# Kernel optimization log

Hardware: AMD Instinct MI355X
Metric: run time of the kernel (lower is better)

Reference implementation:

```python
import jax, jax.numpy as jnp
import numpy as np

B, S, D = 4, 2048, 2048
H, K = 16, 128          # num_heads, intermediate_dim
FINAL = H * K           # 2048
VDIM = 2048             # vector_dim
EPS_LN = 1e-6
EPS_NORM = 1e-30


def setup_inputs() -> dict:
    key = jax.random.key(0)
    ks = jax.random.split(key, 8)
    x = jax.random.normal(ks[0], (B, S, D), dtype=jnp.float32)
    vector = jax.random.normal(ks[1], (B, VDIM), dtype=jnp.float32)
    W_att = jax.random.normal(ks[2], (D, H), dtype=jnp.float32) / np.sqrt(D)
    temperature = jnp.ones((1, 1, H), dtype=jnp.float32)
    W_values = jax.random.normal(ks[3], (D, H, K), dtype=jnp.float32) / np.sqrt(D)
    W_op = jax.random.normal(ks[4], (FINAL, VDIM), dtype=jnp.float32) / np.sqrt(FINAL)
    ff1 = jax.random.normal(ks[5], (VDIM + D, D), dtype=jnp.float32) / np.sqrt(VDIM + D)
    ff1_b = jnp.zeros((1, 1, D), dtype=jnp.float32)
    ff2 = jax.random.normal(ks[6], (D, D), dtype=jnp.float32) / np.sqrt(D)
    ff2_b = jnp.zeros((1, 1, D), dtype=jnp.float32)
    gamma = jnp.ones((D,), dtype=jnp.float32)
    beta = jnp.zeros((D,), dtype=jnp.float32)
    return {"x": x, "vector": vector, "W_att": W_att, "temperature": temperature,
            "W_values": W_values, "W_op": W_op, "ff1": ff1, "ff1_b": ff1_b,
            "ff2": ff2, "ff2_b": ff2_b, "gamma": gamma, "beta": beta}


def reference(x, vector, W_att, temperature, W_values, W_op, ff1, ff1_b, ff2, ff2_b, gamma, beta):
    b, s, d = x.shape
    # attention gate per (query) position -- [B,S,H]
    logits = jnp.matmul(x, W_att)
    logits = logits - jnp.max(logits, axis=-2, keepdims=True)
    w = jnp.exp(logits * temperature)
    # exact collapse of repeat+tril+normalize: A[b,i,j,h] = w[b,i,h]*tril[i,j]
    # denom[b,i,h] = w[b,i,h]*(i+1) + 1e-30  ->  out = coef * causal cumsum of v
    counts = jnp.arange(1, s + 1, dtype=x.dtype)[None, :, None]  # [1,S,1]
    coef = w / (w * counts + EPS_NORM)                            # [B,S,H]
    v = jnp.einsum('bsi,ihk->bshk', x, W_values)                  # [B,S,H,K]
    cum_v = jnp.cumsum(v, axis=1)                                 # prefix-sum over keys
    pooled = (coef[..., None] * cum_v).reshape(b, s, -1)          # [B,S,H*K]
    op = jnp.matmul(pooled, W_op) + vector[:, None, :]            # [B,S,VDIM]
    concat = jnp.concatenate([x, op], axis=-1)                    # [B,S,VDIM+D]
    h = jax.nn.relu(jnp.matmul(concat, ff1) + ff1_b)
    h = jax.nn.relu(jnp.matmul(h, ff2) + ff2_b)
    res = h + x
    mean = jnp.mean(res, axis=-1, keepdims=True)
    cen = res - mean
    var = jnp.mean(cen * cen, axis=-1, keepdims=True)
    return cen / jnp.sqrt(var + EPS_LN) * gamma + beta
```

## Files before the change

### kernel.cpp

```cpp
#include <hip/hip_runtime.h>
#include <stdint.h>

#define B_DIM 4
#define S_DIM 2048
#define D_DIM 2048
#define H_DIM 16
#define M_ROWS (B_DIM * S_DIM)
#define CONCAT_LD 4096
#define NCHUNK 32
#define CHLEN (S_DIM / NCHUNK)

#define BM 128
#define BN 128
#define BK 64

typedef __attribute__((ext_vector_type(8))) __bf16 bf16x8;
typedef __attribute__((ext_vector_type(4))) float f32x4;

__device__ inline unsigned short f2bf(float f) {
  union { float f; unsigned u; } x; x.f = f;
  unsigned r = x.u + 0x7fffu + ((x.u >> 16) & 1u);
  return (unsigned short)(r >> 16);
}
__device__ inline float bf2f(unsigned short s) {
  union { unsigned u; float f; } x; x.u = ((unsigned)s) << 16;
  return x.f;
}

__global__ __launch_bounds__(256) void xconv_logits_kernel(
    const float* __restrict__ x, const float* __restrict__ Watt,
    unsigned short* __restrict__ concat, float* __restrict__ logits) {
  int row = blockIdx.x, t = threadIdx.x;
  const float* xr = x + (size_t)row * D_DIM;
  unsigned short* cr = concat + (size_t)row * CONCAT_LD;
  float p[H_DIM];
#pragma unroll
  for (int h = 0; h < H_DIM; ++h) p[h] = 0.f;
#pragma unroll
  for (int i = 0; i < 8; ++i) {
    int k = t + i * 256;
    float xv = xr[k];
    cr[k] = f2bf(xv);
    const float* wr = Watt + (size_t)k * H_DIM;
#pragma unroll
    for (int h = 0; h < H_DIM; ++h) p[h] += xv * wr[h];
  }
  __shared__ float red[4][H_DIM];
  int l = t & 63, w = t >> 6;
#pragma unroll
  for (int h = 0; h < H_DIM; ++h) {
    float v = p[h];
    for (int off = 32; off; off >>= 1) v += __shfl_down(v, off);
    if (l == 0) red[w][h] = v;
  }
  __syncthreads();
  if (t < H_DIM)
    logits[(size_t)row * H_DIM + t] = red[0][t] + red[1][t] + red[2][t] + red[3][t];
}

__global__ __launch_bounds__(256) void prep_kernel(
    const float* __restrict__ Wval, const float* __restrict__ ff1,
    const float* __restrict__ ff2, const float* __restrict__ Wop,
    unsigned short* __restrict__ wv_t, unsigned short* __restrict__ btff1,
    unsigned short* __restrict__ f1bT, unsigned short* __restrict__ ff2_t,
    unsigned short* __restrict__ wop_bf) {
  int z = blockIdx.z;
  if (z == 4) {
    size_t idx = (((size_t)blockIdx.y * 64 + blockIdx.x) * 256 + threadIdx.x) * 4;
    const float4 v = *(const float4*)(Wop + idx);
    ushort4 o;
    o.x = f2bf(v.x); o.y = f2bf(v.y); o.z = f2bf(v.z); o.w = f2bf(v.w);
    *(ushort4*)(wop_bf + idx) = o;
    return;
  }
  const float* src;
  unsigned short* dst;
  int ldd;
  if (z == 0)      { src = Wval;                        dst = wv_t;  ldd = 2048; }
  else if (z == 1) { src = ff1;                         dst = btff1; ldd = 4096; }
  else if (z == 2) { src = ff1 + (size_t)2048 * 2048;   dst = f1bT;  ldd = 2048; }
  else             { src = ff2;                         dst = ff2_t; ldd = 2048; }
  __shared__ float tile[32][33];
  int c0 = blockIdx.x * 32, r0 = blockIdx.y * 32;
  int tx = threadIdx.x & 31, ty = threadIdx.x >> 5;
#pragma unroll
  for (int i = 0; i < 32; i += 8)
    tile[ty + i][tx] = src[(size_t)(r0 + ty + i) * 2048 + c0 + tx];
  __syncthreads();
#pragma unroll
  for (int i = 0; i < 32; i += 8)
    dst[(size_t)(c0 + ty + i) * ldd + r0 + tx] = f2bf(tile[tx][ty + i]);
}

__global__ __launch_bounds__(256) void coef_kernel(
    const float* __restrict__ logits, const float* __restrict__ temp, float* __restrict__ coef) {
  int b = blockIdx.x >> 4, h = blockIdx.x & 15;
  int t = threadIdx.x;
  const float* lg = logits + (size_t)b * S_DIM * H_DIM + h;
  float mx = -1e30f;
  for (int s = t; s < S_DIM; s += 256) mx = fmaxf(mx, lg[(size_t)s * H_DIM]);
  for (int off = 32; off; off >>= 1) mx = fmaxf(mx, __shfl_down(mx, off));
  __shared__ float red[4];
  if ((t & 63) == 0) red[t >> 6] = mx;
  __syncthreads();
  mx = fmaxf(fmaxf(red[0], red[1]), fmaxf(red[2], red[3]));
  float T = temp[h];
  float* cf = coef + (size_t)b * S_DIM * H_DIM + h;
  for (int s = t; s < S_DIM; s += 256) {
    float w = expf((lg[(size_t)s * H_DIM] - mx) * T);
    cf[(size_t)s * H_DIM] = w / (w * (float)(s + 1) + 1e-30f);
  }
}

__global__ __launch_bounds__(256) void bias2_partial_kernel(
    const float* __restrict__ vector, const float* __restrict__ ff1,
    float* __restrict__ part) {
  int n = blockIdx.x * 256 + threadIdx.x;
  int seg = blockIdx.y, b = blockIdx.z;
  const float* vr = vector + (size_t)b * 2048 + seg * 128;
  const float* fr = ff1 + (size_t)(2048 + seg * 128) * 2048 + n;
  float acc = 0.f;
#pragma unroll 8
  for (int j = 0; j < 128; ++j) acc += vr[j] * fr[(size_t)j * 2048];
  part[((size_t)seg * 4 + b) * 2048 + n] = acc;
}

__global__ __launch_bounds__(256) void bias2_reduce_kernel(
    const float* __restrict__ part, const float* __restrict__ ff1_b,
    float* __restrict__ bias2) {
  int n = blockIdx.x * 256 + threadIdx.x;
  int b = blockIdx.y;
  float acc = ff1_b[n];
#pragma unroll
  for (int s = 0; s < 16; ++s) acc += part[((size_t)s * 4 + b) * 2048 + n];
  bias2[(size_t)b * 2048 + n] = acc;
}

template <int MODE>
__global__ __launch_bounds__(256) void gemm_bt_kernel(
    const unsigned short* __restrict__ A, int lda,
    const unsigned short* __restrict__ Bt, int ldb, int K,
    void* __restrict__ outp, int ldo,
    const float* __restrict__ bias, const float* __restrict__ resid) {
  __shared__ unsigned short As[BM * BK];
  __shared__ unsigned short Bs[BN * BK];
  const int t = threadIdx.x;
  const int w = t >> 6, l = t & 63;
  const int wm = w & 1, wn = w >> 1;
  const int q = l >> 4, ln = l & 15;

  const int L = blockIdx.y * 16 + blockIdx.x;
  const int xcd = L & 7;
  const int W = L >> 3;
  const int bx = W & 15;
  const int by = (W >> 4) * 8 + xcd;
  const int m0 = by * BM, n0 = bx * BN;

  f32x4 acc[4][4];
#pragma unroll
  for (int i = 0; i < 4; ++i)
#pragma unroll
    for (int j = 0; j < 4; ++j) acc[i][j] = {0.f, 0.f, 0.f, 0.f};

  for (int k0 = 0; k0 < K; k0 += BK) {
    __syncthreads();
#pragma unroll
    for (int r = 0; r < 4; ++r) {
      int s = r * 256 + t;
      int row = s >> 3;
      int ch = (s & 7) ^ (row & 7);
      const unsigned short* ga = A + (size_t)(m0 + row) * lda + k0 + ch * 8;
      __builtin_amdgcn_global_load_lds(
          (const __attribute__((address_space(1))) void*)ga,
          (__attribute__((address_space(3))) void*)(As + (r * 256 + w * 64) * 8), 16, 0, 0);
      const unsigned short* gb = Bt + (size_t)(n0 + row) * ldb + k0 + ch * 8;
      __builtin_amdgcn_global_load_lds(
          (const __attribute__((address_space(1))) void*)gb,
          (__attribute__((address_space(3))) void*)(Bs + (r * 256 + w * 64) * 8), 16, 0, 0);
    }
    __syncthreads();
#pragma unroll
    for (int h = 0; h < 2; ++h) {
      bf16x8 af[4], bfr[4];
#pragma unroll
      for (int mt = 0; mt < 4; ++mt) {
        int ar = wm * 64 + mt * 16 + ln;
        af[mt] = *(const bf16x8*)&As[ar * BK + (((h * 4 + q) ^ (ar & 7)) * 8)];
      }
#pragma unroll
      for (int nt = 0; nt < 4; ++nt) {
        int br = wn * 64 + nt * 16 + ln;
        bfr[nt] = *(const bf16x8*)&Bs[br * BK + (((h * 4 + q) ^ (br & 7)) * 8)];
      }
#pragma unroll
      for (int mt = 0; mt < 4; ++mt)
#pragma unroll
        for (int nt = 0; nt < 4; ++nt)
          acc[mt][nt] = __builtin_amdgcn_mfma_f32_16x16x32_bf16(af[mt], bfr[nt], acc[mt][nt], 0, 0, 0);
    }
  }

#pragma unroll
  for (int mt = 0; mt < 4; ++mt) {
#pragma unroll
    for (int i = 0; i < 4; ++i) {
      int row = m0 + wm * 64 + mt * 16 + q * 4 + i;
#pragma unroll
      for (int nt = 0; nt < 4; ++nt) {
        int col = n0 + wn * 64 + nt * 16 + ln;
        float vv = acc[mt][nt][i];
        if (MODE == 2) { vv += bias[(size_t)(row >> 11) * 2048 + col]; vv = fmaxf(vv, 0.f); }
        if (MODE == 4) {
          vv += bias[col]; vv = fmaxf(vv, 0.f);
          vv += resid[(size_t)row * 2048 + col];
          ((float*)outp)[(size_t)row * ldo + col] = vv;
        } else {
          ((unsigned short*)outp)[(size_t)row * ldo + col] = f2bf(vv);
        }
      }
    }
  }
}

#define GLD16(g, s)                                                        \
  __builtin_amdgcn_global_load_lds(                                        \
      (const __attribute__((address_space(1))) void*)(g),                  \
      (__attribute__((address_space(3))) void*)(s), 16, 0, 0)
#define BARX() asm volatile("s_barrier" ::: "memory")
#define VMW8() asm volatile("s_waitcnt vmcnt(8)" ::: "memory")
#define VMW4() asm volatile("s_waitcnt vmcnt(4)" ::: "memory")
#define VMW0() asm volatile("s_waitcnt vmcnt(0)" ::: "memory")

template <int MODE>
__global__ __launch_bounds__(512, 2) void gemm256_kernel(
    const unsigned short* __restrict__ A, int lda,
    const unsigned short* __restrict__ Bt, int ldb, int K,
    void* __restrict__ outp, int ldo,
    const float* __restrict__ bias, const float* __restrict__ resid) {
  __shared__ unsigned short As[2][2][256 * 32];
  __shared__ unsigned short Bs[2][2][256 * 32];
  const int t = threadIdx.x;
  const int wv = t >> 6, l = t & 63;
  const int wm = wv >> 2, wn = wv & 3;
  const int q = l >> 4, ln = l & 15;

  const int L = blockIdx.y * 8 + blockIdx.x;
  const int lin = (L & 7) * 32 + (L >> 3);
  const int m0 = (lin >> 3) * 256, n0 = (lin & 7) * 256;

  const int srow = t >> 2;
  const int scol = (((t & 3) * 16) ^ (((srow >> 1) & 3) << 4)) >> 1;
  const unsigned short* Abase = A + (size_t)(m0 + srow) * lda + scol;
  const unsigned short* Bbase = Bt + (size_t)(n0 + srow) * ldb + scol;
  const size_t astep = (size_t)128 * lda, bstep = (size_t)128 * ldb;
  const int rsel = (q * 8) ^ (((ln >> 1) & 3) << 3);

  f32x4 acc[8][4];
#pragma unroll
  for (int i = 0; i < 8; ++i)
#pragma unroll
    for (int j = 0; j < 4; ++j) acc[i][j] = {0.f, 0.f, 0.f, 0.f};

  auto stageA = [&](int kt, int kh, int buf) {
    const unsigned short* g = Abase + (size_t)kt * 64 + kh * 32;
    GLD16(g, &As[buf][kh][wv * 512]);
    GLD16(g + astep, &As[buf][kh][4096 + wv * 512]);
  };
  auto stageB = [&](int kt, int kh, int buf) {
    const unsigned short* g = Bbase + (size_t)kt * 64 + kh * 32;
    GLD16(g, &Bs[buf][kh][wv * 512]);
    GLD16(g + bstep, &Bs[buf][kh][4096 + wv * 512]);
  };

  bf16x8 a[8], b[2];
  auto loadA = [&](int buf, int h) {
#pragma unroll
    for (int mt = 0; mt < 8; ++mt) {
      int ar = wm * 128 + mt * 16 + ln;
      a[mt] = *(const bf16x8*)&As[buf][h][ar * 32 + rsel];
    }
  };
  auto loadB2 = [&](int buf, int h, int np) {
#pragma unroll
    for (int i = 0; i < 2; ++i) {
      int br = wn * 64 + (np * 2 + i) * 16 + ln;
      b[i] = *(const bf16x8*)&Bs[buf][h][br * 32 + rsel];
    }
  };
  auto mm = [&](int np) {
    __builtin_amdgcn_s_setprio(1);
#pragma unroll
    for (int mt = 0; mt < 8; ++mt)
#pragma unroll
      for (int i = 0; i < 2; ++i)
        acc[mt][np * 2 + i] =
            __builtin_amdgcn_mfma_f32_16x16x32_bf16(a[mt], b[i], acc[mt][np * 2 + i], 0, 0, 0);
    __builtin_amdgcn_s_setprio(0);
  };

  const int NT = K >> 6;
  stageA(0, 0, 0); stageB(0, 0, 0);
  stageA(0, 1, 0); stageB(0, 1, 0);
  stageA(1, 0, 1); stageB(1, 0, 1);
  VMW4();
  BARX();

  for (int tt = 0; tt < NT; ++tt) {
    const int c = tt & 1;
    const int t1 = (tt + 1 == NT) ? 0 : tt + 1;
    const int t2 = (tt + 2 >= NT) ? tt + 2 - NT : tt + 2;
    loadA(c, 0); loadB2(c, 0, 0);
    stageA(t1, 1, c ^ 1);
    BARX();
    mm(0);
    BARX();
    loadB2(c, 0, 1);
    stageB(t1, 1, c ^ 1);
    BARX();
    mm(1);
    VMW8();
    BARX();
    loadA(c, 1); loadB2(c, 1, 0);
    stageA(t2, 0, c);
    BARX();
    mm(0);
    BARX();
    loadB2(c, 1, 1);
    stageB(t2, 0, c);
    BARX();
    mm(1);
    VMW8();
    BARX();
  }
  VMW0();

#pragma unroll
  for (int mt = 0; mt < 8; ++mt) {
#pragma unroll
    for (int i = 0; i < 4; ++i) {
      int row = m0 + wm * 128 + mt * 16 + q * 4 + i;
#pragma unroll
      for (int nt = 0; nt < 4; ++nt) {
        int col = n0 + wn * 64 + nt * 16 + ln;
        float vv = acc[mt][nt][i];
        if (MODE == 2) { vv += bias[(size_t)(row >> 11) * 2048 + col]; vv = fmaxf(vv, 0.f); }
        if (MODE == 4) {
          vv += bias[col]; vv = fmaxf(vv, 0.f);
          vv += resid[(size_t)row * 2048 + col];
          ((float*)outp)[(size_t)row * ldo + col] = vv;
        } else {
          ((unsigned short*)outp)[(size_t)row * ldo + col] = f2bf(vv);
        }
      }
    }
  }
}

__global__ __launch_bounds__(256) void scan_partial_kernel(
    const unsigned short* __restrict__ v, float* __restrict__ csum) {
  int c = blockIdx.x * 256 + threadIdx.x;
  int chunk = blockIdx.y, b = blockIdx.z;
  const unsigned short* p = v + ((size_t)(b * S_DIM + chunk * CHLEN)) * D_DIM + c;
  float s = 0.f;
#pragma unroll 4
  for (int i = 0; i < CHLEN; ++i) s += bf2f(p[(size_t)i * D_DIM]);
  csum[((size_t)b * NCHUNK + chunk) * D_DIM + c] = s;
}

__global__ __launch_bounds__(256) void scan_apply_kernel(
    const unsigned short* __restrict__ v, const float* __restrict__ csum,
    const float* __restrict__ coef, unsigned short* __restrict__ pooled_out) {
  int c = blockIdx.x * 256 + threadIdx.x;
  int chunk = blockIdx.y, b = blockIdx.z;
  int h = c >> 7;
  int row0 = b * S_DIM + chunk * CHLEN;
  const float* cs = csum + (size_t)b * NCHUNK * D_DIM + c;
  float run = 0.f;
  for (int j = 0; j < chunk; ++j) run += cs[(size_t)j * D_DIM];
  const unsigned short* vp = v + (size_t)row0 * D_DIM + c;
  unsigned short* po = pooled_out + (size_t)row0 * CONCAT_LD + c;
  const float* cf = coef + (size_t)row0 * H_DIM + h;
#pragma unroll 4
  for (int i = 0; i < CHLEN; ++i) {
    run += bf2f(vp[(size_t)i * D_DIM]);
    po[(size_t)i * CONCAT_LD] = f2bf(cf[(size_t)i * H_DIM] * run);
  }
}

__global__ __launch_bounds__(256) void ln_kernel(
    float* __restrict__ out, const float* __restrict__ gamma, const float* __restrict__ beta) {
  int row = blockIdx.x, t = threadIdx.x;
  float* pr = out + (size_t)row * D_DIM;
  float vals[8];
  float s = 0.f;
#pragma unroll
  for (int i = 0; i < 8; ++i) { vals[i] = pr[t + i * 256]; s += vals[i]; }
  __shared__ float red[4];
  for (int off = 32; off; off >>= 1) s += __shfl_down(s, off);
  if ((t & 63) == 0) red[t >> 6] = s;
  __syncthreads();
  float mean = (red[0] + red[1] + red[2] + red[3]) * (1.f / D_DIM);
  __syncthreads();
  float c2 = 0.f;
#pragma unroll
  for (int i = 0; i < 8; ++i) { float c = vals[i] - mean; c2 += c * c; }
  for (int off = 32; off; off >>= 1) c2 += __shfl_down(c2, off);
  if ((t & 63) == 0) red[t >> 6] = c2;
  __syncthreads();
  float var = (red[0] + red[1] + red[2] + red[3]) * (1.f / D_DIM);
  float rstd = rsqrtf(var + 1e-6f);
#pragma unroll
  for (int i = 0; i < 8; ++i) {
    int col = t + i * 256;
    pr[col] = (vals[i] - mean) * rstd * gamma[col] + beta[col];
  }
}

extern "C" void kernel_launch(void* const* d_in, const int* in_sizes, int n_in,
                              void* d_out, int out_size, void* d_ws, size_t ws_size,
                              hipStream_t stream) {
  const float* x      = (const float*)d_in[0];
  const float* vector = (const float*)d_in[1];
  const float* W_att  = (const float*)d_in[2];
  const float* temp   = (const float*)d_in[3];
  const float* W_val  = (const float*)d_in[4];
  const float* W_op   = (const float*)d_in[5];
  const float* ff1    = (const float*)d_in[6];
  const float* ff1_b  = (const float*)d_in[7];
  const float* ff2    = (const float*)d_in[8];
  const float* ff2_b  = (const float*)d_in[9];
  const float* gamma  = (const float*)d_in[10];
  const float* beta   = (const float*)d_in[11];
  float* out = (float*)d_out;

  char* ws = (char*)d_ws;
  auto alloc = [&](size_t bytes) {
    char* p = ws; ws += (bytes + 255) & ~(size_t)255; return p;
  };
  unsigned short* concat = (unsigned short*)alloc((size_t)M_ROWS * CONCAT_LD * 2);
  unsigned short* wv_t   = (unsigned short*)alloc((size_t)2048 * 2048 * 2);
  unsigned short* btff1  = (unsigned short*)alloc((size_t)2048 * 4096 * 2);
  unsigned short* f1bT   = (unsigned short*)alloc((size_t)2048 * 2048 * 2);
  unsigned short* wop_bf = (unsigned short*)alloc((size_t)2048 * 2048 * 2);
  unsigned short* ff2_t  = (unsigned short*)alloc((size_t)2048 * 2048 * 2);
  unsigned short* vbuf   = (unsigned short*)alloc((size_t)M_ROWS * 2048 * 2);
  unsigned short* h1     = (unsigned short*)alloc((size_t)M_ROWS * 2048 * 2);
  float* logits = (float*)alloc((size_t)M_ROWS * H_DIM * 4);
  float* coef   = (float*)alloc((size_t)M_ROWS * H_DIM * 4);
  float* csum   = (float*)alloc((size_t)B_DIM * NCHUNK * D_DIM * 4);
  float* part   = (float*)alloc((size_t)16 * 4 * 2048 * 4);
  float* bias2  = (float*)alloc((size_t)4 * 2048 * 4);

  prep_kernel<<<dim3(64, 64, 5), 256, 0, stream>>>(
      W_val, ff1, ff2, W_op, wv_t, btff1, f1bT, ff2_t, wop_bf);
  xconv_logits_kernel<<<M_ROWS, 256, 0, stream>>>(x, W_att, concat, logits);
  coef_kernel<<<B_DIM * H_DIM, 256, 0, stream>>>(logits, temp, coef);
  gemm_bt_kernel<1><<<dim3(16, 16), 256, 0, stream>>>(
      f1bT, 2048, wop_bf, 2048, 2048, btff1 + 2048, 4096, nullptr, nullptr);
  bias2_partial_kernel<<<dim3(8, 16, 4), 256, 0, stream>>>(vector, ff1, part);
  bias2_reduce_kernel<<<dim3(8, 4), 256, 0, stream>>>(part, ff1_b, bias2);
  gemm256_kernel<1><<<dim3(8, 32), 512, 0, stream>>>(
      concat, CONCAT_LD, wv_t, 2048, 2048, vbuf, 2048, nullptr, nullptr);
  scan_partial_kernel<<<dim3(8, NCHUNK, B_DIM), 256, 0, stream>>>(vbuf, csum);
  scan_apply_kernel<<<dim3(8, NCHUNK, B_DIM), 256, 0, stream>>>(vbuf, csum, coef, concat + 2048);
  gemm256_kernel<2><<<dim3(8, 32), 512, 0, stream>>>(
      concat, CONCAT_LD, btff1, 4096, 4096, h1, 2048, bias2, nullptr);
  gemm256_kernel<4><<<dim3(8, 32), 512, 0, stream>>>(
      h1, 2048, ff2_t, 2048, 2048, out, 2048, ff2_b, x);
  ln_kernel<<<M_ROWS, 256, 0, stream>>>(out, gamma, beta);
}
```

Measured before the change: 651.4 us.

## Vectorize memory access in elementwise, scan, transpose and layernorm kernels

Widens global loads and stores across the auxiliary kernels. The x-conversion/logits kernel now handles four rows per block with float4 loads and reuses each W_att row across them. The transpose prep writes ushort2 pairs over 64-row tiles, and the scan kernels process eight bf16 columns per thread with 128-bit accesses and twice as many chunks. Layernorm uses float4 loads and stores. The aim is to cut memory-instruction count and uncoalesced narrow accesses in these bandwidth-bound steps, at the cost of fewer blocks in the scans and more registers per thread.

```diff
diff --git a/kernel.cpp b/kernel.cpp
--- a/kernel.cpp
+++ b/kernel.cpp
@@ -7,7 +7,7 @@
 #define H_DIM 16
 #define M_ROWS (B_DIM * S_DIM)
 #define CONCAT_LD 4096
-#define NCHUNK 32
+#define NCHUNK 64
 #define CHLEN (S_DIM / NCHUNK)
 
 #define BM 128
@@ -26,36 +26,63 @@
   union { unsigned u; float f; } x; x.u = ((unsigned)s) << 16;
   return x.f;
 }
+__device__ inline float bfLo(unsigned u) {
+  union { unsigned x; float f; } c; c.x = u << 16; return c.f;
+}
+__device__ inline float bfHi(unsigned u) {
+  union { unsigned x; float f; } c; c.x = u & 0xffff0000u; return c.f;
+}
 
 __global__ __launch_bounds__(256) void xconv_logits_kernel(
     const float* __restrict__ x, const float* __restrict__ Watt,
     unsigned short* __restrict__ concat, float* __restrict__ logits) {
-  int row = blockIdx.x, t = threadIdx.x;
-  const float* xr = x + (size_t)row * D_DIM;
-  unsigned short* cr = concat + (size_t)row * CONCAT_LD;
-  float p[H_DIM];
-#pragma unroll
-  for (int h = 0; h < H_DIM; ++h) p[h] = 0.f;
-#pragma unroll
-  for (int i = 0; i < 8; ++i) {
-    int k = t + i * 256;
-    float xv = xr[k];
-    cr[k] = f2bf(xv);
-    const float* wr = Watt + (size_t)k * H_DIM;
-#pragma unroll
-    for (int h = 0; h < H_DIM; ++h) p[h] += xv * wr[h];
-  }
-  __shared__ float red[4][H_DIM];
+  int r0 = blockIdx.x * 4, t = threadIdx.x;
+  float p[4][H_DIM];
+#pragma unroll
+  for (int r = 0; r < 4; ++r)
+#pragma unroll
+    for (int h = 0; h < H_DIM; ++h) p[r][h] = 0.f;
+#pragma unroll
+  for (int i = 0; i < 2; ++i) {
+    int k = t * 4 + i * 1024;
+    float4 xv[4];
+#pragma unroll
+    for (int r = 0; r < 4; ++r) {
+      xv[r] = *(const float4*)(x + (size_t)(r0 + r) * D_DIM + k);
+      ushort4 o;
+      o.x = f2bf(xv[r].x); o.y = f2bf(xv[r].y); o.z = f2bf(xv[r].z); o.w = f2bf(xv[r].w);
+      *(ushort4*)(concat + (size_t)(r0 + r) * CONCAT_LD + k) = o;
+    }
+#pragma unroll
+    for (int kk = 0; kk < 4; ++kk) {
+      const float* w = Watt + (size_t)(k + kk) * H_DIM;
+      float wr[H_DIM];
+#pragma unroll
+      for (int h = 0; h < H_DIM; ++h) wr[h] = w[h];
+#pragma unroll
+      for (int r = 0; r < 4; ++r) {
+        float xs = (kk == 0) ? xv[r].x : (kk == 1) ? xv[r].y : (kk == 2) ? xv[r].z : xv[r].w;
+#pragma unroll
+        for (int h = 0; h < H_DIM; ++h) p[r][h] += xs * wr[h];
+      }
+    }
+  }
+  __shared__ float red[4][4][H_DIM];
   int l = t & 63, w = t >> 6;
 #pragma unroll
-  for (int h = 0; h < H_DIM; ++h) {
-    float v = p[h];
-    for (int off = 32; off; off >>= 1) v += __shfl_down(v, off);
-    if (l == 0) red[w][h] = v;
-  }
+  for (int r = 0; r < 4; ++r)
+#pragma unroll
+    for (int h = 0; h < H_DIM; ++h) {
+      float v = p[r][h];
+      for (int off = 32; off; off >>= 1) v += __shfl_down(v, off);
+      if (l == 0) red[w][r][h] = v;
+    }
   __syncthreads();
-  if (t < H_DIM)
-    logits[(size_t)row * H_DIM + t] = red[0][t] + red[1][t] + red[2][t] + red[3][t];
+  if (t < 64) {
+    int r = t >> 4, h = t & 15;
+    logits[(size_t)(r0 + r) * H_DIM + h] =
+        red[0][r][h] + red[1][r][h] + red[2][r][h] + red[3][r][h];
+  }
 }
 
 __global__ __launch_bounds__(256) void prep_kernel(
@@ -64,13 +91,16 @@
     unsigned short* __restrict__ wv_t, unsigned short* __restrict__ btff1,
     unsigned short* __restrict__ f1bT, unsigned short* __restrict__ ff2_t,
     unsigned short* __restrict__ wop_bf) {
-  int z = blockIdx.z;
+  int z = blockIdx.z, t = threadIdx.x;
   if (z == 4) {
-    size_t idx = (((size_t)blockIdx.y * 64 + blockIdx.x) * 256 + threadIdx.x) * 4;
-    const float4 v = *(const float4*)(Wop + idx);
-    ushort4 o;
-    o.x = f2bf(v.x); o.y = f2bf(v.y); o.z = f2bf(v.z); o.w = f2bf(v.w);
-    *(ushort4*)(wop_bf + idx) = o;
+    size_t idx = (((size_t)blockIdx.y * 64 + blockIdx.x) * 256 + t) * 8;
+    const float4 v0 = *(const float4*)(Wop + idx);
+    const float4 v1 = *(const float4*)(Wop + idx + 4);
+    ushort4 a, b;
+    a.x = f2bf(v0.x); a.y = f2bf(v0.y); a.z = f2bf(v0.z); a.w = f2bf(v0.w);
+    b.x = f2bf(v1.x); b.y = f2bf(v1.y); b.z = f2bf(v1.z); b.w = f2bf(v1.w);
+    *(ushort4*)(wop_bf + idx) = a;
+    *(ushort4*)(wop_bf + idx + 4) = b;
     return;
   }
   const float* src;
@@ -80,16 +110,22 @@
   else if (z == 1) { src = ff1;                         dst = btff1; ldd = 4096; }
   else if (z == 2) { src = ff1 + (size_t)2048 * 2048;   dst = f1bT;  ldd = 2048; }
   else             { src = ff2;                         dst = ff2_t; ldd = 2048; }
-  __shared__ float tile[32][33];
-  int c0 = blockIdx.x * 32, r0 = blockIdx.y * 32;
-  int tx = threadIdx.x & 31, ty = threadIdx.x >> 5;
-#pragma unroll
-  for (int i = 0; i < 32; i += 8)
+  __shared__ float tile[64][33];
+  int c0 = blockIdx.x * 32, r0 = blockIdx.y * 64;
+  int tx = t & 31, ty = t >> 5;
+#pragma unroll
+  for (int i = 0; i < 64; i += 8)
     tile[ty + i][tx] = src[(size_t)(r0 + ty + i) * 2048 + c0 + tx];
   __syncthreads();
-#pragma unroll
-  for (int i = 0; i < 32; i += 8)
-    dst[(size_t)(c0 + ty + i) * ldd + r0 + tx] = f2bf(tile[tx][ty + i]);
+  int sx = t & 31, sy = t >> 5;
+#pragma unroll
+  for (int j = 0; j < 32; j += 8) {
+    int c = c0 + sy + j;
+    ushort2 o;
+    o.x = f2bf(tile[sx * 2][sy + j]);
+    o.y = f2bf(tile[sx * 2 + 1][sy + j]);
+    *(ushort2*)(dst + (size_t)c * ldd + r0 + sx * 2) = o;
+  }
 }
 
 __global__ __launch_bounds__(256) void coef_kernel(
@@ -358,32 +394,57 @@
 
 __global__ __launch_bounds__(256) void scan_partial_kernel(
     const unsigned short* __restrict__ v, float* __restrict__ csum) {
-  int c = blockIdx.x * 256 + threadIdx.x;
-  int chunk = blockIdx.y, b = blockIdx.z;
-  const unsigned short* p = v + ((size_t)(b * S_DIM + chunk * CHLEN)) * D_DIM + c;
-  float s = 0.f;
-#pragma unroll 4
-  for (int i = 0; i < CHLEN; ++i) s += bf2f(p[(size_t)i * D_DIM]);
-  csum[((size_t)b * NCHUNK + chunk) * D_DIM + c] = s;
+  int chunk = blockIdx.x, b = blockIdx.y;
+  int c0 = threadIdx.x * 8;
+  const unsigned short* p = v + ((size_t)(b * S_DIM + chunk * CHLEN)) * D_DIM + c0;
+  float s[8];
+#pragma unroll
+  for (int j = 0; j < 8; ++j) s[j] = 0.f;
+  for (int i = 0; i < CHLEN; ++i) {
+    uint4 u = *(const uint4*)(p + (size_t)i * D_DIM);
+    s[0] += bfLo(u.x); s[1] += bfHi(u.x);
+    s[2] += bfLo(u.y); s[3] += bfHi(u.y);
+    s[4] += bfLo(u.z); s[5] += bfHi(u.z);
+    s[6] += bfLo(u.w); s[7] += bfHi(u.w);
+  }
+  float* cs = csum + ((size_t)b * NCHUNK + chunk) * D_DIM + c0;
+  float4 o0 = {s[0], s[1], s[2], s[3]}, o1 = {s[4], s[5], s[6], s[7]};
+  *(float4*)cs = o0;
+  *(float4*)(cs + 4) = o1;
 }
 
 __global__ __launch_bounds__(256) void scan_apply_kernel(
     const unsigned short* __restrict__ v, const float* __restrict__ csum,
     const float* __restrict__ coef, unsigned short* __restrict__ pooled_out) {
-  int c = blockIdx.x * 256 + threadIdx.x;
-  int chunk = blockIdx.y, b = blockIdx.z;
-  int h = c >> 7;
+  int chunk = blockIdx.x, b = blockIdx.y;
+  int c0 = threadIdx.x * 8;
+  const float* cs = csum + (size_t)b * NCHUNK * D_DIM + c0;
+  float run[8];
+#pragma unroll
+  for (int j = 0; j < 8; ++j) run[j] = 0.f;
+  for (int j = 0; j < chunk; ++j) {
+    float4 a = *(const float4*)(cs + (size_t)j * D_DIM);
+    float4 d = *(const float4*)(cs + (size_t)j * D_DIM + 4);
+    run[0] += a.x; run[1] += a.y; run[2] += a.z; run[3] += a.w;
+    run[4] += d.x; run[5] += d.y; run[6] += d.z; run[7] += d.w;
+  }
   int row0 = b * S_DIM + chunk * CHLEN;
-  const float* cs = csum + (size_t)b * NCHUNK * D_DIM + c;
-  float run = 0.f;
-  for (int j = 0; j < chunk; ++j) run += cs[(size_t)j * D_DIM];
-  const unsigned short* vp = v + (size_t)row0 * D_DIM + c;
-  unsigned short* po = pooled_out + (size_t)row0 * CONCAT_LD + c;
-  const float* cf = coef + (size_t)row0 * H_DIM + h;
-#pragma unroll 4
+  const unsigned short* vp = v + (size_t)row0 * D_DIM + c0;
+  unsigned short* po = pooled_out + (size_t)row0 * CONCAT_LD + c0;
+  const float* cf = coef + (size_t)row0 * H_DIM + (c0 >> 7);
   for (int i = 0; i < CHLEN; ++i) {
-    run += bf2f(vp[(size_t)i * D_DIM]);
-    po[(size_t)i * CONCAT_LD] = f2bf(cf[(size_t)i * H_DIM] * run);
+    uint4 u = *(const uint4*)(vp + (size_t)i * D_DIM);
+    run[0] += bfLo(u.x); run[1] += bfHi(u.x);
+    run[2] += bfLo(u.y); run[3] += bfHi(u.y);
+    run[4] += bfLo(u.z); run[5] += bfHi(u.z);
+    run[6] += bfLo(u.w); run[7] += bfHi(u.w);
+    float cv = cf[(size_t)i * H_DIM];
+    uint4 o;
+    o.x = (unsigned)f2bf(cv * run[0]) | ((unsigned)f2bf(cv * run[1]) << 16);
+    o.y = (unsigned)f2bf(cv * run[2]) | ((unsigned)f2bf(cv * run[3]) << 16);
+    o.z = (unsigned)f2bf(cv * run[4]) | ((unsigned)f2bf(cv * run[5]) << 16);
+    o.w = (unsigned)f2bf(cv * run[6]) | ((unsigned)f2bf(cv * run[7]) << 16);
+    *(uint4*)(po + (size_t)i * CONCAT_LD) = o;
   }
 }
 
@@ -391,10 +452,10 @@
     float* __restrict__ out, const float* __restrict__ gamma, const float* __restrict__ beta) {
   int row = blockIdx.x, t = threadIdx.x;
   float* pr = out + (size_t)row * D_DIM;
-  float vals[8];
-  float s = 0.f;
-#pragma unroll
-  for (int i = 0; i < 8; ++i) { vals[i] = pr[t + i * 256]; s += vals[i]; }
+  int c = t * 4;
+  float4 va = *(const float4*)(pr + c);
+  float4 vb = *(const float4*)(pr + c + 1024);
+  float s = va.x + va.y + va.z + va.w + vb.x + vb.y + vb.z + vb.w;
   __shared__ float red[4];
   for (int off = 32; off; off >>= 1) s += __shfl_down(s, off);
   if ((t & 63) == 0) red[t >> 6] = s;
@@ -402,18 +463,31 @@
   float mean = (red[0] + red[1] + red[2] + red[3]) * (1.f / D_DIM);
   __syncthreads();
   float c2 = 0.f;
-#pragma unroll
-  for (int i = 0; i < 8; ++i) { float c = vals[i] - mean; c2 += c * c; }
+  {
+    float d;
+    d = va.x - mean; c2 += d * d; d = va.y - mean; c2 += d * d;
+    d = va.z - mean; c2 += d * d; d = va.w - mean; c2 += d * d;
+    d = vb.x - mean; c2 += d * d; d = vb.y - mean; c2 += d * d;
+    d = vb.z - mean; c2 += d * d; d = vb.w - mean; c2 += d * d;
+  }
   for (int off = 32; off; off >>= 1) c2 += __shfl_down(c2, off);
   if ((t & 63) == 0) red[t >> 6] = c2;
   __syncthreads();
   float var = (red[0] + red[1] + red[2] + red[3]) * (1.f / D_DIM);
   float rstd = rsqrtf(var + 1e-6f);
-#pragma unroll
-  for (int i = 0; i < 8; ++i) {
-    int col = t + i * 256;
-    pr[col] = (vals[i] - mean) * rstd * gamma[col] + beta[col];
-  }
+  float4 ga = *(const float4*)(gamma + c), ba = *(const float4*)(beta + c);
+  float4 gb = *(const float4*)(gamma + c + 1024), bb = *(const float4*)(beta + c + 1024);
+  float4 oa, ob;
+  oa.x = (va.x - mean) * rstd * ga.x + ba.x;
+  oa.y = (va.y - mean) * rstd * ga.y + ba.y;
+  oa.z = (va.z - mean) * rstd * ga.z + ba.z;
+  oa.w = (va.w - mean) * rstd * ga.w + ba.w;
+  ob.x = (vb.x - mean) * rstd * gb.x + bb.x;
+  ob.y = (vb.y - mean) * rstd * gb.y + bb.y;
+  ob.z = (vb.z - mean) * rstd * gb.z + bb.z;
+  ob.w = (vb.w - mean) * rstd * gb.w + bb.w;
+  *(float4*)(pr + c) = oa;
+  *(float4*)(pr + c + 1024) = ob;
 }
 
 extern "C" void kernel_launch(void* const* d_in, const int* in_sizes, int n_in,
@@ -451,9 +525,9 @@
   float* part   = (float*)alloc((size_t)16 * 4 * 2048 * 4);
   float* bias2  = (float*)alloc((size_t)4 * 2048 * 4);
 
-  prep_kernel<<<dim3(64, 64, 5), 256, 0, stream>>>(
+  prep_kernel<<<dim3(64, 32, 5), 256, 0, stream>>>(
       W_val, ff1, ff2, W_op, wv_t, btff1, f1bT, ff2_t, wop_bf);
-  xconv_logits_kernel<<<M_ROWS, 256, 0, stream>>>(x, W_att, concat, logits);
+  xconv_logits_kernel<<<M_ROWS / 4, 256, 0, stream>>>(x, W_att, concat, logits);
   coef_kernel<<<B_DIM * H_DIM, 256, 0, stream>>>(logits, temp, coef);
   gemm_bt_kernel<1><<<dim3(16, 16), 256, 0, stream>>>(
       f1bT, 2048, wop_bf, 2048, 2048, btff1 + 2048, 4096, nullptr, nullptr);
@@ -461,8 +535,8 @@
   bias2_reduce_kernel<<<dim3(8, 4), 256, 0, stream>>>(part, ff1_b, bias2);
   gemm256_kernel<1><<<dim3(8, 32), 512, 0, stream>>>(
       concat, CONCAT_LD, wv_t, 2048, 2048, vbuf, 2048, nullptr, nullptr);
-  scan_partial_kernel<<<dim3(8, NCHUNK, B_DIM), 256, 0, stream>>>(vbuf, csum);
-  scan_apply_kernel<<<dim3(8, NCHUNK, B_DIM), 256, 0, stream>>>(vbuf, csum, coef, concat + 2048);
+  scan_partial_kernel<<<dim3(NCHUNK, B_DIM), 256, 0, stream>>>(vbuf, csum);
+  scan_apply_kernel<<<dim3(NCHUNK, B_DIM), 256, 0, stream>>>(vbuf, csum, coef, concat + 2048);
   gemm256_kernel<2><<<dim3(8, 32), 512, 0, stream>>>(
       concat, CONCAT_LD, btff1, 4096, 4096, h1, 2048, bias2, nullptr);
   gemm256_kernel<4><<<dim3(8, 32), 512, 0, stream>>>(
```

New measurement: 627.6 us. -3.7%, faster.
